# Performance work log

Measured on AMD Instinct MI355X. Metric: run time of the kernel, lower is better.

The kernel has to match this reference:

```python
import jax, jax.numpy as jnp
import numpy as np

USER_NUM = 200000
ITEM_NUM = 100000
N_NODES = USER_NUM + ITEM_NUM
EMB = 64
N_EDGES = 4800000
N_LAYERS = 3


def setup_inputs() -> dict:
    key = jax.random.key(0)
    k1, k2, k3, k4, k5 = jax.random.split(key, 5)
    user_emb = jax.random.normal(k1, (USER_NUM, EMB), dtype=jnp.float32) * 0.1
    item_emb = jax.random.normal(k2, (ITEM_NUM, EMB), dtype=jnp.float32) * 0.1
    # COO normalized adjacency: out[src] += val * x[dst]
    edge_src = jax.random.randint(k3, (N_EDGES,), 0, N_NODES, dtype=jnp.int32)
    edge_dst = jax.random.randint(k4, (N_EDGES,), 0, N_NODES, dtype=jnp.int32)
    # values like D^{-1/2} A D^{-1/2} entries: small positive
    edge_val = jax.random.uniform(k5, (N_EDGES,), dtype=jnp.float32) * (1.0 / 16.0)
    return {"user_emb": user_emb, "item_emb": item_emb, "edge_val": edge_val,
            "edge_src": edge_src, "edge_dst": edge_dst}


def _spmm(edge_src, edge_dst, edge_val, x):
    # sparse (N,N) @ dense (N,d): gather rows, scale, scatter-add by src
    gathered = x[edge_dst] * edge_val[:, None]  # [E, d]
    return jax.ops.segment_sum(gathered, edge_src, num_segments=N_NODES)


def reference(user_emb, item_emb, edge_val, edge_src, edge_dst):
    ego = jnp.concatenate([user_emb, item_emb], axis=0)  # [N, d]
    acc = jnp.zeros_like(ego)
    for _ in range(N_LAYERS):
        ego = _spmm(edge_src, edge_dst, edge_val, ego)
        acc = acc + ego
    all_emb = acc / N_LAYERS  # mean over layer outputs
    return all_emb[:USER_NUM], all_emb[USER_NUM:]
```

## Files before the change

### kernel.cpp

```cpp
#include <hip/hip_runtime.h>

#define USER_NUM 200000
#define ITEM_NUM 100000
#define N_NODES  300000
#define EMB      64
#define N_EDGES  4800000
#define N_LAYERS 3

#define BKT_LOG   10
#define BKT_NODES (1 << BKT_LOG)
#define N_BKT     ((N_NODES + BKT_NODES - 1) >> BKT_LOG)
#define BKT_CAP   18432

#define PA_U      16
#define PA_THR    512
#define PA_EDGES  (PA_THR * PA_U)
#define PA_NB     ((N_EDGES + PA_EDGES - 1) / PA_EDGES)

#define PB_THR    1024
#define PB_RPT    (BKT_CAP / PB_THR)
#define PB_LDS    (BKT_CAP * 8 + BKT_NODES * 4 + BKT_NODES * 4)

typedef int   v2i __attribute__((ext_vector_type(2)));
typedef float v4f __attribute__((ext_vector_type(4)));
typedef _Float16 v8h __attribute__((ext_vector_type(8)));


__global__ __launch_bounds__(PA_THR) void partA_kernel(
    const int* __restrict__ esrc, const int* __restrict__ edst,
    const float* __restrict__ eval, int* __restrict__ bktCursor,
    int2* __restrict__ stage)
{
    __shared__ int lhist[N_BKT];
    __shared__ int lbase[N_BKT];
    for (int i = threadIdx.x; i < N_BKT; i += PA_THR) lhist[i] = 0;
    __syncthreads();

    int base = blockIdx.x * PA_EDGES + threadIdx.x;
    int s[PA_U], d[PA_U], r[PA_U];
    float v[PA_U];
    #pragma unroll
    for (int i = 0; i < PA_U; ++i) {
        int e = base + i * PA_THR;
        if (e < N_EDGES) {
            s[i] = esrc[e];
            d[i] = edst[e];
            v[i] = eval[e];
            r[i] = atomicAdd(&lhist[s[i] >> BKT_LOG], 1);
        } else {
            s[i] = -1;
        }
    }
    __syncthreads();
    for (int i = threadIdx.x; i < N_BKT; i += PA_THR)
        lbase[i] = atomicAdd(&bktCursor[i], lhist[i]);
    __syncthreads();
    #pragma unroll
    for (int i = 0; i < PA_U; ++i) {
        if (s[i] >= 0) {
            int bkt = s[i] >> BKT_LOG;
            int pl  = lbase[bkt] + r[i];
            if (pl < BKT_CAP) {
                int packed = ((s[i] & (BKT_NODES - 1)) << 19) | d[i];
                stage[(size_t)bkt * BKT_CAP + pl] =
                    make_int2(packed, __float_as_int(v[i]));
            }
        }
    }
}

__global__ __launch_bounds__(512) void scanB_kernel(
    const int* __restrict__ bktCursor, int* __restrict__ bktBase,
    int* __restrict__ rowptr)
{
    __shared__ int lds[512];
    int t = threadIdx.x;
    int c = 0;
    if (t < N_BKT) { c = bktCursor[t]; if (c > BKT_CAP) c = BKT_CAP; }
    lds[t] = c;
    __syncthreads();
    for (int off = 1; off < 512; off <<= 1) {
        int v = (t >= off) ? lds[t - off] : 0;
        __syncthreads();
        lds[t] += v;
        __syncthreads();
    }
    int excl = (t == 0) ? 0 : lds[t - 1];
    if (t < N_BKT)  bktBase[t] = excl;
    if (t == N_BKT) bktBase[t] = lds[N_BKT - 1];
    if (t == 0)     rowptr[N_NODES] = lds[N_BKT - 1];
}

__global__ __launch_bounds__(PB_THR) void partB_kernel(
    const int2* __restrict__ stage, const int* __restrict__ bktBase,
    int* __restrict__ rowptr, int2* __restrict__ edges_s)
{
    extern __shared__ char smem[];
    v2i* lbuf = (v2i*)smem;
    int* lcnt = (int*)(smem + BKT_CAP * 8);
    int* lcur = (int*)(smem + BKT_CAP * 8 + BKT_NODES * 4);

    int b  = blockIdx.x;
    int lo = b << BKT_LOG;
    int hi = lo + BKT_NODES; if (hi > N_NODES) hi = N_NODES;
    int gbase = bktBase[b];
    int cnt   = bktBase[b + 1] - gbase;
    int t = threadIdx.x;

    v2i er[PB_RPT];
    #pragma unroll
    for (int i = 0; i < PB_RPT; ++i) {
        int idx = t + i * PB_THR;
        er[i] = (idx < cnt)
              ? ((const v2i*)stage)[(size_t)b * BKT_CAP + idx]
              : (v2i){0, 0};
    }
    lcnt[t] = 0;
    __syncthreads();
    #pragma unroll
    for (int i = 0; i < PB_RPT; ++i) {
        int idx = t + i * PB_THR;
        if (idx < cnt) atomicAdd(&lcnt[((unsigned)er[i].x) >> 19], 1);
    }
    __syncthreads();
    for (int off = 1; off < BKT_NODES; off <<= 1) {
        int v = (t >= off) ? lcnt[t - off] : 0;
        __syncthreads();
        lcnt[t] += v;
        __syncthreads();
    }
    int excl = (t == 0) ? 0 : lcnt[t - 1];
    lcur[t] = excl;
    if (lo + t < hi) rowptr[lo + t] = gbase + excl;
    __syncthreads();
    #pragma unroll
    for (int i = 0; i < PB_RPT; ++i) {
        int idx = t + i * PB_THR;
        if (idx < cnt) {
            int ls = ((unsigned)er[i].x) >> 19;
            int p  = atomicAdd(&lcur[ls], 1);
            v2i out; out.x = er[i].x & 0x7FFFF; out.y = er[i].y;
            lbuf[p] = out;
        }
    }
    __syncthreads();
    for (int e = t; e < cnt; e += PB_THR)
        __builtin_nontemporal_store(lbuf[e], (v2i*)(edges_s + gbase + e));
}

__global__ __launch_bounds__(256) void convert_kernel(
    const float* __restrict__ userp, const float* __restrict__ itemp,
    _Float16* __restrict__ xh)
{
    const size_t UN  = (size_t)USER_NUM * EMB / 8;
    const size_t TOT = (size_t)N_NODES * EMB / 8;
    size_t i = (size_t)blockIdx.x * 256 + threadIdx.x;
    if (i >= TOT) return;
    const float* src = (i < UN) ? (userp + i * 8) : (itemp + (i - UN) * 8);
    v4f a = __builtin_nontemporal_load((const v4f*)src);
    v4f b = __builtin_nontemporal_load((const v4f*)src + 1);
    v8h h;
    #pragma unroll
    for (int k = 0; k < 4; ++k) { h[k] = (_Float16)a[k]; h[4 + k] = (_Float16)b[k]; }
    __builtin_nontemporal_store(h, (v8h*)(xh + i * 8));
}

__global__ __launch_bounds__(256) void spmm_csr(
    const int2*     __restrict__ edges_s,
    const int*      __restrict__ rowptr,
    const _Float16* __restrict__ xg,
    _Float16*       __restrict__ yout,
    const _Float16* __restrict__ y1,
    const _Float16* __restrict__ y2,
    float*          __restrict__ out,
    int final_)
{
    int wid  = __builtin_amdgcn_readfirstlane(
                   (int)((blockIdx.x * blockDim.x + threadIdx.x) >> 6));
    int lane = threadIdx.x & 63;
    if (wid >= N_NODES) return;

    int start = rowptr[wid];
    int end   = rowptr[wid + 1];

    float a0 = 0.0f, a1 = 0.0f;
    for (int base = start; base < end; base += 64) {
        int m = end - base;
        if (m > 64) m = 64;
        v2i e;
        if (lane < m) e = __builtin_nontemporal_load((const v2i*)(edges_s + base + lane));
        else          { e.x = 0; e.y = 0; }
        int groups = (m + 15) >> 4;
        for (int g = 0; g < groups; ++g) {
            int j = g << 4;
            float p[16], vv[16];
            #pragma unroll
            for (int k = 0; k < 16; ++k) {
                int d  = __builtin_amdgcn_readlane(e.x, j + k);
                vv[k]  = __int_as_float(__builtin_amdgcn_readlane(e.y, j + k));
                p[k]   = (float)xg[(size_t)d * EMB + lane];
            }
            #pragma unroll
            for (int k = 0; k < 16; k += 2) {
                a0 += vv[k]     * p[k];
                a1 += vv[k + 1] * p[k + 1];
            }
        }
    }

    float a = a0 + a1;
    size_t o = (size_t)wid * EMB + lane;
    if (!final_) {
        __builtin_nontemporal_store((_Float16)a, &yout[o]);
    } else {
        float s1 = (float)__builtin_nontemporal_load(&y1[o]);
        float s2 = (float)__builtin_nontemporal_load(&y2[o]);
        __builtin_nontemporal_store((a + s1 + s2) * (1.0f / 3.0f), &out[o]);
    }
}


extern "C" void kernel_launch(void* const* d_in, const int* in_sizes, int n_in,
                              void* d_out, int out_size, void* d_ws, size_t ws_size,
                              hipStream_t stream)
{
    const float* user_emb = (const float*)d_in[0];
    const float* item_emb = (const float*)d_in[1];
    const float* edge_val = (const float*)d_in[2];
    const int*   edge_src = (const int*)  d_in[3];
    const int*   edge_dst = (const int*)  d_in[4];
    float* out = (float*)d_out;

    const size_t nodeh_bytes = (size_t)N_NODES * EMB * 2;

    char* ws = (char*)d_ws;
    _Float16* xh   = (_Float16*)ws;               ws += nodeh_bytes;
    _Float16* yh_a = (_Float16*)ws;               ws += nodeh_bytes;
    _Float16* yh_b = (_Float16*)ws;               ws += nodeh_bytes;
    int2*  edges_s  = (int2*)ws;                  ws += (size_t)N_EDGES * 8;
    int*   rowptr   = (int*)ws;                   ws += (size_t)(N_NODES + 1) * 4;
    int*   bktCur   = (int*)ws;                   ws += N_BKT * 4;
    int*   bktBase  = (int*)ws;                   ws += (N_BKT + 1) * 4;

    int2* stage = (int2*)yh_a;

    hipMemsetAsync(bktCur, 0, N_BKT * 4, stream);
    convert_kernel<<<(int)(((size_t)N_NODES * EMB / 8 + 255) / 256), 256, 0,
                     stream>>>(user_emb, item_emb, xh);
    partA_kernel<<<PA_NB, PA_THR, 0, stream>>>(edge_src, edge_dst, edge_val,
                                               bktCur, stage);
    scanB_kernel<<<1, 512, 0, stream>>>(bktCur, bktBase, rowptr);
    partB_kernel<<<N_BKT, PB_THR, PB_LDS, stream>>>(stage, bktBase,
                                                    rowptr, edges_s);

    const int spmm_blocks = (N_NODES * 64 + 255) / 256;
    spmm_csr<<<spmm_blocks, 256, 0, stream>>>(edges_s, rowptr, xh,
                                              yh_a, nullptr, nullptr, nullptr, 0);
    spmm_csr<<<spmm_blocks, 256, 0, stream>>>(edges_s, rowptr, yh_a,
                                              yh_b, nullptr, nullptr, nullptr, 0);
    spmm_csr<<<spmm_blocks, 256, 0, stream>>>(edges_s, rowptr, yh_b,
                                              nullptr, yh_a, yh_b, out, 1);
}
```

Baseline: 630.9 us.

## Process two CSR rows per wavefront with half-wave lanes loading packed fp16 pairs

Each 64-lane wavefront of the SpMM kernel now handles two adjacent rows. Each 32-lane half owns one row and each lane loads two fp16 features with a single 32-bit load. Edge indices are broadcast with shuffles instead of readlane, and outputs are written as packed pairs. This aims to halve the wavefront count and the per-row overhead while widening gather loads. The cost is divergence when the two rows have different degrees, plus shuffle (ds_bpermute) overhead in place of scalar readlane.

```diff
diff --git a/kernel.cpp b/kernel.cpp
--- a/kernel.cpp
+++ b/kernel.cpp
@@ -21,9 +21,11 @@
 #define PB_RPT    (BKT_CAP / PB_THR)
 #define PB_LDS    (BKT_CAP * 8 + BKT_NODES * 4 + BKT_NODES * 4)
 
-typedef int   v2i __attribute__((ext_vector_type(2)));
-typedef float v4f __attribute__((ext_vector_type(4)));
+typedef int      v2i __attribute__((ext_vector_type(2)));
+typedef float    v4f __attribute__((ext_vector_type(4)));
+typedef float    v2f __attribute__((ext_vector_type(2)));
 typedef _Float16 v8h __attribute__((ext_vector_type(8)));
+typedef _Float16 v2h __attribute__((ext_vector_type(2)));
 
 
 __global__ __launch_bounds__(PA_THR) void partA_kernel(
@@ -175,47 +177,58 @@
     float*          __restrict__ out,
     int final_)
 {
-    int wid  = __builtin_amdgcn_readfirstlane(
-                   (int)((blockIdx.x * blockDim.x + threadIdx.x) >> 6));
+    int wpair = __builtin_amdgcn_readfirstlane(
+                    (int)((blockIdx.x * blockDim.x + threadIdx.x) >> 6));
+    int r0 = wpair * 2;
+    if (r0 >= N_NODES) return;
     int lane = threadIdx.x & 63;
-    if (wid >= N_NODES) return;
-
-    int start = rowptr[wid];
-    int end   = rowptr[wid + 1];
+    int h = lane >> 5;
+    int c = lane & 31;
+
+    int s0 = rowptr[r0];
+    int s1 = rowptr[r0 + 1];
+    int s2 = rowptr[r0 + 2];
+    int m0 = s1 - s0;
+    int m1 = s2 - s1;
+    int mmax   = (m0 > m1) ? m0 : m1;
+    int startH = h ? s1 : s0;
+    int mH     = h ? m1 : m0;
 
     float a0 = 0.0f, a1 = 0.0f;
-    for (int base = start; base < end; base += 64) {
-        int m = end - base;
-        if (m > 64) m = 64;
-        v2i e;
-        if (lane < m) e = __builtin_nontemporal_load((const v2i*)(edges_s + base + lane));
-        else          { e.x = 0; e.y = 0; }
-        int groups = (m + 15) >> 4;
-        for (int g = 0; g < groups; ++g) {
-            int j = g << 4;
-            float p[16], vv[16];
+    for (int base = 0; base < mmax; base += 32) {
+        v2i e = {0, 0};
+        if (base + c < mH)
+            e = __builtin_nontemporal_load((const v2i*)(edges_s + startH + base + c));
+        int rem = mmax - base; if (rem > 32) rem = 32;
+        for (int j = 0; j < rem; j += 8) {
+            unsigned pk[8]; float vv[8];
             #pragma unroll
-            for (int k = 0; k < 16; ++k) {
-                int d  = __builtin_amdgcn_readlane(e.x, j + k);
-                vv[k]  = __int_as_float(__builtin_amdgcn_readlane(e.y, j + k));
-                p[k]   = (float)xg[(size_t)d * EMB + lane];
+            for (int k = 0; k < 8; ++k) {
+                int sl = (j + k) | (h << 5);
+                int d  = __shfl(e.x, sl);
+                vv[k]  = __int_as_float(__shfl(e.y, sl));
+                pk[k]  = *(const unsigned*)(xg + (size_t)d * EMB + c * 2);
             }
             #pragma unroll
-            for (int k = 0; k < 16; k += 2) {
-                a0 += vv[k]     * p[k];
-                a1 += vv[k + 1] * p[k + 1];
+            for (int k = 0; k < 8; ++k) {
+                v2h ph = __builtin_bit_cast(v2h, pk[k]);
+                a0 += vv[k] * (float)ph[0];
+                a1 += vv[k] * (float)ph[1];
             }
         }
     }
 
-    float a = a0 + a1;
-    size_t o = (size_t)wid * EMB + lane;
+    size_t ro = (size_t)(r0 + h) * EMB + c * 2;
     if (!final_) {
-        __builtin_nontemporal_store((_Float16)a, &yout[o]);
+        v2h o2; o2[0] = (_Float16)a0; o2[1] = (_Float16)a1;
+        __builtin_nontemporal_store(o2, (v2h*)(yout + ro));
     } else {
-        float s1 = (float)__builtin_nontemporal_load(&y1[o]);
-        float s2 = (float)__builtin_nontemporal_load(&y2[o]);
-        __builtin_nontemporal_store((a + s1 + s2) * (1.0f / 3.0f), &out[o]);
+        v2h q1 = __builtin_nontemporal_load((const v2h*)(y1 + ro));
+        v2h q2 = __builtin_nontemporal_load((const v2h*)(y2 + ro));
+        v2f o;
+        o[0] = (a0 + (float)q1[0] + (float)q2[0]) * (1.0f / 3.0f);
+        o[1] = (a1 + (float)q1[1] + (float)q2[1]) * (1.0f / 3.0f);
+        __builtin_nontemporal_store(o, (v2f*)(out + ro));
     }
 }
 
@@ -253,7 +266,8 @@
     partB_kernel<<<N_BKT, PB_THR, PB_LDS, stream>>>(stage, bktBase,
                                                     rowptr, edges_s);
 
-    const int spmm_blocks = (N_NODES * 64 + 255) / 256;
+    const int npairs = N_NODES / 2;
+    const int spmm_blocks = (npairs * 64 + 255) / 256;
     spmm_csr<<<spmm_blocks, 256, 0, stream>>>(edges_s, rowptr, xh,
                                               yh_a, nullptr, nullptr, nullptr, 0);
     spmm_csr<<<spmm_blocks, 256, 0, stream>>>(edges_s, rowptr, yh_a,
```

Result: faster. 543.6 us (-13.8%).
